# Optimization experiments

Hardware: AMD Instinct MI355X
Metric: run time of the kernel (lower is better)

## Reference

```python
import jax, jax.numpy as jnp
import numpy as np

T_MAX = 201  # TEXT_MAX_LEN
HID = 512
VOCAB = 100  # NUM_CHAR
BATCH = 2048


def setup_inputs() -> dict:
    key = jax.random.key(0)
    ks = jax.random.split(key, 8)
    s = 0.05  # keep gates in a sane range
    return {
        "feat": jax.random.normal(ks[0], (BATCH, HID), jnp.float32),      # resnet pooler_output
        "W_ih": jax.random.normal(ks[1], (3 * HID, HID), jnp.float32) * s,  # torch weight_ih_l0 (r,z,n)
        "W_hh": jax.random.normal(ks[2], (3 * HID, HID), jnp.float32) * s,
        "b_ih": jax.random.normal(ks[3], (3 * HID,), jnp.float32) * s,
        "b_hh": jax.random.normal(ks[4], (3 * HID,), jnp.float32) * s,
        "W_proj": jax.random.normal(ks[5], (VOCAB, HID), jnp.float32) * s,
        "b_proj": jax.random.normal(ks[6], (VOCAB,), jnp.float32) * s,
        "embed": jax.random.normal(ks[7], (VOCAB, HID), jnp.float32) * s,
        "sos": 0,
    }


def _gru_cell(x, h, W_ih, W_hh, b_ih, b_hh):
    # torch GRU cell: gates ordered (reset, update, new)
    gi = x @ W_ih.T + b_ih            # [B, 3H]
    gh = h @ W_hh.T + b_hh            # [B, 3H]
    i_r, i_z, i_n = jnp.split(gi, 3, axis=-1)
    h_r, h_z, h_n = jnp.split(gh, 3, axis=-1)
    r = jax.nn.sigmoid(i_r + h_r)
    z = jax.nn.sigmoid(i_z + h_z)
    n = jnp.tanh(i_n + r * h_n)
    return (1.0 - z) * n + z * h


def reference(feat, W_ih, W_hh, b_ih, b_hh, W_proj, b_proj, embed, sos):
    B = feat.shape[0]
    # start token embedding broadcast over batch
    x0 = jnp.broadcast_to(embed[sos], (B, HID))
    h0 = feat  # encoder features initialize the GRU hidden state

    def step(carry, _):
        h, x = carry
        h = _gru_cell(x, h, W_ih, W_hh, b_ih, b_hh)
        logits = h @ W_proj.T + b_proj          # [B, V]
        pred = jnp.argmax(logits, axis=-1)      # greedy decode
        x_next = embed[pred]                    # [B, H]
        return (h, x_next), logits

    _, logits_tbv = jax.lax.scan(step, (h0, x0), None, length=T_MAX)  # [T, B, V]
    # outputs.permute(0, 2, 1): [B, V, T]
    return jnp.transpose(logits_tbv, (1, 2, 0))
```

## Files before the change

### kernel.cpp

```cpp
#include <hip/hip_runtime.h>
#include <cmath>

#define HID   512
#define VOCAB 100
#define G3    1536
#define GEXT  1664
#define NT    104
#define TMAX  201
#define ROWS  8
#define BLOCK 1024
#define NWG   256
#define TPW   13
#define GHS   1672

typedef __bf16 bf16x8 __attribute__((ext_vector_type(8)));
typedef float  f32x4  __attribute__((ext_vector_type(4)));
typedef unsigned int u32x4 __attribute__((ext_vector_type(4)));

#define SZ_WPK   (NT * 16 * 2 * 64 * 8)
#define FBASE    (SZ_WPK / 2)
#define OFF_EIH  FBASE
#define SZ_EIH   (VOCAB * G3)
#define OFF_WIHT (OFF_EIH + SZ_EIH)
#define SZ_WIHT  (HID * G3)
#define OFF_BEXT (OFF_WIHT + SZ_WIHT)

__global__ void prep_kernel(const float* __restrict__ W_ih,
                            const float* __restrict__ b_hh,
                            const float* __restrict__ b_proj,
                            float* __restrict__ ws)
{
  int idx = blockIdx.x * 256 + threadIdx.x;
  if (idx < SZ_WIHT) {
    int k = idx / G3, j = idx - k * G3;
    ws[OFF_WIHT + idx] = W_ih[j * HID + k];
  } else if (idx < SZ_WIHT + GEXT) {
    int j = idx - SZ_WIHT;
    float v = 0.f;
    if (j < G3)              v = b_hh[j];
    else if (j < G3 + VOCAB) v = b_proj[j - G3];
    ws[OFF_BEXT + j] = v;
  }
}

__global__ void pack_kernel(const float* __restrict__ W_hh,
                            const float* __restrict__ W_proj,
                            __bf16* __restrict__ wpk)
{
  int idx = blockIdx.x * 256 + threadIdx.x;
  if (idx >= NT * 16 * 64 * 8) return;
  int j    = idx & 7;
  int lane = (idx >> 3) & 63;
  int ks   = (idx >> 9) & 15;
  int c    = idx >> 13;
  int col  = c * 16 + (lane & 15);
  int k    = ks * 32 + (lane >> 4) * 8 + j;
  float w = 0.f;
  if (col < G3)              w = W_hh[col * HID + k];
  else if (col < G3 + VOCAB) w = W_proj[(col - G3) * HID + k];
  __bf16 hi = (__bf16)w;
  __bf16 lo = (__bf16)(w - (float)hi);
  int base = (((c * 16 + ks) * 2) * 64 + lane) * 8 + j;
  wpk[base]       = hi;
  wpk[base + 512] = lo;
}

__global__ void eih_kernel(const float* __restrict__ embed,
                           const float* __restrict__ b_ih,
                           float* __restrict__ ws)
{
  int v = blockIdx.x / 6;
  int j = (blockIdx.x % 6) * 256 + threadIdx.x;
  const float* WihT = ws + OFF_WIHT;
  const float* e = embed + v * HID;
  float acc = b_ih[j];
  for (int k = 0; k < HID; ++k)
    acc = fmaf(WihT[k * G3 + j], e[k], acc);
  ws[OFF_EIH + v * G3 + j] = acc;
}

#define GLD4(F0, F1, F2, F3, P)                                   \
  asm volatile("global_load_dwordx4 %0, %4, off\n\t"              \
               "global_load_dwordx4 %1, %4, off offset:1024\n\t"  \
               "global_load_dwordx4 %2, %4, off offset:2048\n\t"  \
               "global_load_dwordx4 %3, %4, off offset:3072"      \
               : "=&v"(F0), "=&v"(F1), "=&v"(F2), "=&v"(F3)       \
               : "v"(P))

#define VMWAIT(N)                                 \
  do { asm volatile("s_waitcnt vmcnt(" #N ")");   \
       __builtin_amdgcn_sched_barrier(0); } while (0)

#define BC(X) __builtin_bit_cast(bf16x8, X)

#define MFMA4(ACC, Q0, Q1, Q2, Q3, A0, A1)                                      \
  do {                                                                          \
    ACC = __builtin_amdgcn_mfma_f32_16x16x32_bf16(A0, BC(Q0), ACC, 0, 0, 0);    \
    ACC = __builtin_amdgcn_mfma_f32_16x16x32_bf16(A0, BC(Q1), ACC, 0, 0, 0);    \
    ACC = __builtin_amdgcn_mfma_f32_16x16x32_bf16(A1, BC(Q2), ACC, 0, 0, 0);    \
    ACC = __builtin_amdgcn_mfma_f32_16x16x32_bf16(A1, BC(Q3), ACC, 0, 0, 0);    \
  } while (0)

#define FOLDWRITE(ACC, TILE)                                      \
  do {                                                            \
    int colw_ = (TILE) * 16 + (lane & 15);                        \
    float vs_[4];                                                 \
    _Pragma("unroll")                                             \
    for (int i_ = 0; i_ < 4; ++i_)                                \
      vs_[i_] = ACC[i_] + __shfl_xor(ACC[i_], 32, 64);            \
    if (lane < 32) {                                              \
      int r0_ = (lane >> 4) * 4;                                  \
      _Pragma("unroll")                                           \
      for (int i_ = 0; i_ < 4; ++i_)                              \
        ghW[r0_ + i_][colw_] = vs_[i_];                           \
    }                                                             \
  } while (0)

__global__ __launch_bounds__(BLOCK) void decode_kernel(
    const float* __restrict__ feat,
    const int* __restrict__ sos,
    const float* __restrict__ ws,
    const __bf16* __restrict__ wpk,
    float* __restrict__ out)
{
  __shared__ __align__(16) char hab[16 * 1024];
  __shared__ float ghA[ROWS][GHS];
  __shared__ float ghB[ROWS][GHS];
  __shared__ int   pred_lds[ROWS];

  const float* __restrict__ EIH  = ws + OFF_EIH;
  const float* __restrict__ bext = ws + OFF_BEXT;

  const int tid  = threadIdx.x;
  const int lane = tid & 63;
  const int wv   = tid >> 6;
  const int half = wv >> 3;
  const int wt   = wv & 7;
  const int b0   = blockIdx.x * ROWS;
  const int u    = tid & (HID - 1);
  const int rb   = (tid >> 9) * 4;

  float (*ghW)[GHS] = half ? ghB : ghA;

  float h[4];
  #pragma unroll
  for (int rr = 0; rr < 4; ++rr) {
    int r = rb + rr;
    float f = feat[(size_t)(b0 + r) * HID + u];
    h[rr] = f;
    __bf16 hi = (__bf16)f;
    __bf16 lo = (__bf16)(f - (float)hi);
    unsigned so = ((unsigned)(u * 2)) ^ (((unsigned)(r & 7)) << 4);
    *(__bf16*)(hab + (r << 10) + so)       = hi;
    *(__bf16*)(hab + ((r + 8) << 10) + so) = lo;
  }
  if (tid < ROWS) pred_lds[tid] = sos[0];
  __syncthreads();

  const float gbr = bext[u], gbz = bext[HID + u], gbn = bext[2 * HID + u];
  const int sr = tid / VOCAB, sv = tid - sr * VOCAB;
  float* outp = nullptr; float outb = 0.f;
  if (tid < ROWS * VOCAB) {
    outp = out + ((size_t)(b0 + sr) * VOCAB + sv) * TMAX;
    outb = bext[G3 + sv];
  }
  const float ab0 = (lane < VOCAB)      ? bext[G3 + lane]      : 0.f;
  const float ab1 = (lane + 64 < VOCAB) ? bext[G3 + 64 + lane] : 0.f;

  const int      arow = lane & 15;
  const unsigned ag   = (unsigned)((lane >> 4) << 4);
  const unsigned axor = ((unsigned)(arow & 7)) << 4;
  const char* ha = hab + (arow << 10);

  const char* const wbase = (const char*)wpk
      + (size_t)(wt * TPW) * 32768 + (size_t)half * 16384 + (size_t)lane * 16;

  for (int t = 0; t <= TMAX; ++t) {
    bf16x8 afr0, afr1, afr2, afr3, afr4, afr5, afr6, afr7;
    {
      const unsigned kb = (unsigned)(half * 8);
      afr0 = *(const bf16x8*)(ha + ((((kb + 0) << 6) + ag) ^ axor));
      afr1 = *(const bf16x8*)(ha + ((((kb + 1) << 6) + ag) ^ axor));
      afr2 = *(const bf16x8*)(ha + ((((kb + 2) << 6) + ag) ^ axor));
      afr3 = *(const bf16x8*)(ha + ((((kb + 3) << 6) + ag) ^ axor));
      afr4 = *(const bf16x8*)(ha + ((((kb + 4) << 6) + ag) ^ axor));
      afr5 = *(const bf16x8*)(ha + ((((kb + 5) << 6) + ag) ^ axor));
      afr6 = *(const bf16x8*)(ha + ((((kb + 6) << 6) + ag) ^ axor));
      afr7 = *(const bf16x8*)(ha + ((((kb + 7) << 6) + ag) ^ axor));
    }

    int tt0 = 0;
    bool active = true;
    if (t == TMAX) { if (wt == 7) tt0 = 5; else active = false; }

    if (active) {
      u32x4 qa0, qa1, qa2, qa3;
      u32x4 qb0, qb1, qb2, qb3;
      const char* bp = wbase + (size_t)tt0 * 32768;

      GLD4(qa0, qa1, qa2, qa3, bp);

      for (int tt = tt0; tt < TPW; ++tt) {
        f32x4 acc = {0.f, 0.f, 0.f, 0.f};
        GLD4(qb0, qb1, qb2, qb3, bp + 4096);
        VMWAIT(4);
        MFMA4(acc, qa0, qa1, qa2, qa3, afr0, afr1);
        GLD4(qa0, qa1, qa2, qa3, bp + 8192);
        VMWAIT(4);
        MFMA4(acc, qb0, qb1, qb2, qb3, afr2, afr3);
        GLD4(qb0, qb1, qb2, qb3, bp + 12288);
        VMWAIT(4);
        MFMA4(acc, qa0, qa1, qa2, qa3, afr4, afr5);
        if (tt + 1 < TPW) {
          GLD4(qa0, qa1, qa2, qa3, bp + 32768);
          VMWAIT(4);
        } else {
          VMWAIT(0);
        }
        MFMA4(acc, qb0, qb1, qb2, qb3, afr6, afr7);
        FOLDWRITE(acc, wt * TPW + tt);
        bp += 32768;
      }
    }
    __syncthreads();

    if (t >= 1) {
      if (tid < ROWS * VOCAB) {
        float lg = ghA[sr][G3 + sv] + ghB[sr][G3 + sv] + outb;
        __builtin_nontemporal_store(lg, outp + (t - 1));
      }
      if (t < TMAX && wv < ROWS) {
        float v0 = (lane < VOCAB)
                   ? ghA[wv][G3 + lane] + ghB[wv][G3 + lane] + ab0 : -1e30f;
        float v1 = (lane + 64 < VOCAB)
                   ? ghA[wv][G3 + 64 + lane] + ghB[wv][G3 + 64 + lane] + ab1 : -1e30f;
        float bv; int bi;
        if (v0 >= v1) { bv = v0; bi = lane; } else { bv = v1; bi = lane + 64; }
        #pragma unroll
        for (int off = 32; off >= 1; off >>= 1) {
          float ov = __shfl_xor(bv, off);
          int   oi = __shfl_xor(bi, off);
          if (ov > bv || (ov == bv && oi < bi)) { bv = ov; bi = oi; }
        }
        if (lane == 0) pred_lds[wv] = bi;
      }
    }
    __syncthreads();

    if (t < TMAX) {
      #pragma unroll
      for (int rr = 0; rr < 4; ++rr) {
        int r = rb + rr;
        const float* eb = EIH + (size_t)pred_lds[r] * G3;
        float srg = eb[u]       + gbr + ghA[r][u]       + ghB[r][u];
        float szg = eb[HID + u] + gbz + ghA[r][HID + u] + ghB[r][HID + u];
        float hn  = ghA[r][2 * HID + u] + ghB[r][2 * HID + u] + gbn;
        float rg = 1.f / (1.f + expf(-srg));
        float zg = 1.f / (1.f + expf(-szg));
        float ng = tanhf(eb[2 * HID + u] + rg * hn);
        h[rr] = (1.f - zg) * ng + zg * h[rr];
        __bf16 hi = (__bf16)h[rr];
        __bf16 lo = (__bf16)(h[rr] - (float)hi);
        unsigned so = ((unsigned)(u * 2)) ^ (((unsigned)(r & 7)) << 4);
        *(__bf16*)(hab + (r << 10) + so)       = hi;
        *(__bf16*)(hab + ((r + 8) << 10) + so) = lo;
      }
    }
    __syncthreads();
  }
}

extern "C" void kernel_launch(void* const* d_in, const int* in_sizes, int n_in,
                              void* d_out, int out_size, void* d_ws, size_t ws_size,
                              hipStream_t stream)
{
  const float* feat   = (const float*)d_in[0];
  const float* W_ih   = (const float*)d_in[1];
  const float* W_hh   = (const float*)d_in[2];
  const float* b_ih   = (const float*)d_in[3];
  const float* b_hh   = (const float*)d_in[4];
  const float* W_proj = (const float*)d_in[5];
  const float* b_proj = (const float*)d_in[6];
  const float* embed  = (const float*)d_in[7];
  const int*   sos    = (const int*)d_in[8];

  float*  wsf = (float*)d_ws;
  __bf16* wpk = (__bf16*)d_ws;
  float*  out = (float*)d_out;

  const int prep_total = SZ_WIHT + GEXT;
  prep_kernel<<<(prep_total + 255) / 256, 256, 0, stream>>>(W_ih, b_hh, b_proj, wsf);
  pack_kernel<<<(NT * 16 * 64 * 8 + 255) / 256, 256, 0, stream>>>(W_hh, W_proj, wpk);
  eih_kernel<<<600, 256, 0, stream>>>(embed, b_ih, wsf);
  decode_kernel<<<NWG, BLOCK, 0, stream>>>(feat, sos, wsf, wpk, out);
}
```

Measured before the change: 6.347 ms.

## Compute argmax redundantly per wave, drop a barrier, fast activations, rotate weight tiles

Every wave now computes the argmax for its own four rows in registers instead of 8 waves writing pred to LDS, which removes one __syncthreads per timestep. Sigmoid and tanh use __expf and hardware reciprocal instead of libm expf/tanhf. The tile order over the streamed weights is rotated per workgroup, so different blocks read different weight tiles at the same time and L2/HBM channel contention drops. The trade-offs are redundant argmax work (4x shuffles per wave) and slightly lower activation accuracy, which could flip greedy argmax ties.

```diff
diff --git a/kernel.cpp b/kernel.cpp
--- a/kernel.cpp
+++ b/kernel.cpp
@@ -116,6 +116,15 @@
     }                                                             \
   } while (0)
 
+__device__ __forceinline__ float fsigm(float x) {
+  return __builtin_amdgcn_rcpf(1.f + __expf(-x));
+}
+__device__ __forceinline__ float ftanh(float x) {
+  float e2 = __expf(-2.f * fabsf(x));
+  float t  = (1.f - e2) * __builtin_amdgcn_rcpf(1.f + e2);
+  return copysignf(t, x);
+}
+
 __global__ __launch_bounds__(BLOCK) void decode_kernel(
     const float* __restrict__ feat,
     const int* __restrict__ sos,
@@ -126,7 +135,6 @@
   __shared__ __align__(16) char hab[16 * 1024];
   __shared__ float ghA[ROWS][GHS];
   __shared__ float ghB[ROWS][GHS];
-  __shared__ int   pred_lds[ROWS];
 
   const float* __restrict__ EIH  = ws + OFF_EIH;
   const float* __restrict__ bext = ws + OFF_BEXT;
@@ -139,22 +147,24 @@
   const int b0   = blockIdx.x * ROWS;
   const int u    = tid & (HID - 1);
   const int rb   = (tid >> 9) * 4;
+  const int rot  = blockIdx.x % TPW;
 
   float (*ghW)[GHS] = half ? ghB : ghA;
 
   float h[4];
+  int   pred[4];
   #pragma unroll
   for (int rr = 0; rr < 4; ++rr) {
     int r = rb + rr;
     float f = feat[(size_t)(b0 + r) * HID + u];
     h[rr] = f;
+    pred[rr] = sos[0];
     __bf16 hi = (__bf16)f;
     __bf16 lo = (__bf16)(f - (float)hi);
     unsigned so = ((unsigned)(u * 2)) ^ (((unsigned)(r & 7)) << 4);
     *(__bf16*)(hab + (r << 10) + so)       = hi;
     *(__bf16*)(hab + ((r + 8) << 10) + so) = lo;
   }
-  if (tid < ROWS) pred_lds[tid] = sos[0];
   __syncthreads();
 
   const float gbr = bext[u], gbz = bext[HID + u], gbn = bext[2 * HID + u];
@@ -189,18 +199,19 @@
       afr7 = *(const bf16x8*)(ha + ((((kb + 7) << 6) + ag) ^ axor));
     }
 
-    int tt0 = 0;
+    int tstart = 0, rot_eff = rot;
     bool active = true;
-    if (t == TMAX) { if (wt == 7) tt0 = 5; else active = false; }
+    if (t == TMAX) { if (wt == 7) { tstart = 5; rot_eff = 0; } else active = false; }
 
     if (active) {
       u32x4 qa0, qa1, qa2, qa3;
       u32x4 qb0, qb1, qb2, qb3;
-      const char* bp = wbase + (size_t)tt0 * 32768;
+      int tl = tstart + rot_eff; if (tl >= TPW) tl -= TPW;
+      const char* bp = wbase + (size_t)tl * 32768;
 
       GLD4(qa0, qa1, qa2, qa3, bp);
 
-      for (int tt = tt0; tt < TPW; ++tt) {
+      for (int tt = tstart; tt < TPW; ++tt) {
         f32x4 acc = {0.f, 0.f, 0.f, 0.f};
         GLD4(qb0, qb1, qb2, qb3, bp + 4096);
         VMWAIT(4);
@@ -211,15 +222,17 @@
         GLD4(qb0, qb1, qb2, qb3, bp + 12288);
         VMWAIT(4);
         MFMA4(acc, qa0, qa1, qa2, qa3, afr4, afr5);
+        int tln = tl + 1; if (tln >= TPW) tln -= TPW;
+        const char* bpn = wbase + (size_t)tln * 32768;
         if (tt + 1 < TPW) {
-          GLD4(qa0, qa1, qa2, qa3, bp + 32768);
+          GLD4(qa0, qa1, qa2, qa3, bpn);
           VMWAIT(4);
         } else {
           VMWAIT(0);
         }
         MFMA4(acc, qb0, qb1, qb2, qb3, afr6, afr7);
-        FOLDWRITE(acc, wt * TPW + tt);
-        bp += 32768;
+        FOLDWRITE(acc, wt * TPW + tl);
+        bp = bpn; tl = tln;
       }
     }
     __syncthreads();
@@ -229,35 +242,38 @@
         float lg = ghA[sr][G3 + sv] + ghB[sr][G3 + sv] + outb;
         __builtin_nontemporal_store(lg, outp + (t - 1));
       }
-      if (t < TMAX && wv < ROWS) {
-        float v0 = (lane < VOCAB)
-                   ? ghA[wv][G3 + lane] + ghB[wv][G3 + lane] + ab0 : -1e30f;
-        float v1 = (lane + 64 < VOCAB)
-                   ? ghA[wv][G3 + 64 + lane] + ghB[wv][G3 + 64 + lane] + ab1 : -1e30f;
-        float bv; int bi;
-        if (v0 >= v1) { bv = v0; bi = lane; } else { bv = v1; bi = lane + 64; }
+      if (t < TMAX) {
         #pragma unroll
-        for (int off = 32; off >= 1; off >>= 1) {
-          float ov = __shfl_xor(bv, off);
-          int   oi = __shfl_xor(bi, off);
-          if (ov > bv || (ov == bv && oi < bi)) { bv = ov; bi = oi; }
+        for (int rr = 0; rr < 4; ++rr) {
+          int row = rb + rr;
+          float v0 = (lane < VOCAB)
+                     ? ghA[row][G3 + lane] + ghB[row][G3 + lane] + ab0 : -1e30f;
+          float v1 = (lane + 64 < VOCAB)
+                     ? ghA[row][G3 + 64 + lane] + ghB[row][G3 + 64 + lane] + ab1 : -1e30f;
+          float bv; int bi;
+          if (v0 >= v1) { bv = v0; bi = lane; } else { bv = v1; bi = lane + 64; }
+          #pragma unroll
+          for (int off = 32; off >= 1; off >>= 1) {
+            float ov = __shfl_xor(bv, off);
+            int   oi = __shfl_xor(bi, off);
+            if (ov > bv || (ov == bv && oi < bi)) { bv = ov; bi = oi; }
+          }
+          pred[rr] = bi;
         }
-        if (lane == 0) pred_lds[wv] = bi;
       }
     }
-    __syncthreads();
 
     if (t < TMAX) {
       #pragma unroll
       for (int rr = 0; rr < 4; ++rr) {
         int r = rb + rr;
-        const float* eb = EIH + (size_t)pred_lds[r] * G3;
+        const float* eb = EIH + (size_t)pred[rr] * G3;
         float srg = eb[u]       + gbr + ghA[r][u]       + ghB[r][u];
         float szg = eb[HID + u] + gbz + ghA[r][HID + u] + ghB[r][HID + u];
         float hn  = ghA[r][2 * HID + u] + ghB[r][2 * HID + u] + gbn;
-        float rg = 1.f / (1.f + expf(-srg));
-        float zg = 1.f / (1.f + expf(-szg));
-        float ng = tanhf(eb[2 * HID + u] + rg * hn);
+        float rg = fsigm(srg);
+        float zg = fsigm(szg);
+        float ng = ftanh(eb[2 * HID + u] + rg * hn);
         h[rr] = (1.f - zg) * ng + zg * h[rr];
         __bf16 hi = (__bf16)h[rr];
         __bf16 lo = (__bf16)(h[rr] - (float)hi);
```

Measured after the change: 6.047 ms. -4.7%, faster.
